# Kernel tuning notes

Measured on AMD Instinct MI355X. Metric: run time of the kernel, lower is better.

## Reference

```python
import jax, jax.numpy as jnp
import numpy as np

B, S, D, H = 2, 2048, 1024, 16
DK = D // H


def setup_inputs() -> dict:
    key = jax.random.key(0)
    ks = jax.random.split(key, 11)
    sc = 0.02
    return {
        "q": jax.random.normal(ks[0], (B, S, D), jnp.float32),
        "k": jax.random.normal(ks[1], (B, S, D), jnp.float32),
        "v": jax.random.normal(ks[2], (B, S, D), jnp.float32),
        "mask": jnp.ones((1, 1, S, S), jnp.int32),
        "w_q": jax.random.normal(ks[3], (D, D), jnp.float32) * sc,
        "b_q": jnp.zeros((D,), jnp.float32),
        "w_k": jax.random.normal(ks[4], (D, D), jnp.float32) * sc,
        "b_k": jnp.zeros((D,), jnp.float32),
        "w_v": jax.random.normal(ks[5], (D, D), jnp.float32) * sc,
        "b_v": jnp.zeros((D,), jnp.float32),
        "w_o": jax.random.normal(ks[6], (D, D), jnp.float32) * sc,
        "b_o": jnp.zeros((D,), jnp.float32),
    }


def reference(q, k, v, mask, w_q, b_q, w_k, b_k, w_v, b_v, w_o, b_o):
    # projections (torch Linear: x @ W.T + b)
    Q = q @ w_q.T + b_q
    K = k @ w_k.T + b_k
    V = v @ w_v.T + b_v
    # [B,S,D] -> [B,H,S,DK]
    Q = Q.reshape(B, S, H, DK).transpose(0, 2, 1, 3)
    K = K.reshape(B, S, H, DK).transpose(0, 2, 1, 3)
    V = V.reshape(B, S, H, DK).transpose(0, 2, 1, 3)
    scores = jnp.einsum('bhqd,bhkd->bhqk', Q, K) / jnp.sqrt(jnp.float32(DK))
    scores = jnp.where(mask == 0, jnp.float32(-1e9), scores)
    attn = jax.nn.softmax(scores, axis=-1)  # dropout p=0.0 -> identity
    X = jnp.einsum('bhqk,bhkd->bhqd', attn, V)
    X = X.transpose(0, 2, 1, 3).reshape(B, S, D)
    return X @ w_o.T + b_o
```

## Files before the change

### kernel.cpp

```cpp
#include <hip/hip_runtime.h>
#include <cstdint>
#include <cstddef>


typedef __attribute__((ext_vector_type(8))) short short8;
typedef __attribute__((ext_vector_type(4))) float float4v;
typedef __attribute__((ext_vector_type(4))) unsigned short us4;

#define DEV __device__ __forceinline__
#define MFMA16(a, b, c) __builtin_amdgcn_mfma_f32_16x16x32_bf16((a), (b), (c), 0, 0, 0)

DEV unsigned short f2bf(float f) {
  union { float f; unsigned u; } c; c.f = f;
  unsigned u = c.u + 0x7fffu + ((c.u >> 16) & 1u);
  return (unsigned short)(u >> 16);
}

DEV void async16(const void* g, void* l) {
  __builtin_amdgcn_global_load_lds(
      (__attribute__((address_space(1))) void*)(uintptr_t)g,
      (__attribute__((address_space(3))) void*)l, 16, 0, 0);
}

struct CvtJob { const float* src; unsigned short* dst; int n; int mode; };
struct CvtArgs { CvtJob job[8]; };

__global__ __launch_bounds__(256) void cvt_bf16_kernel(CvtArgs args) {
  CvtJob j = args.job[blockIdx.y];
  int i = (blockIdx.x * 256 + threadIdx.x) * 8;
  if (i >= j.n) return;
  if (j.mode == 0) {
    float4v a = *(const float4v*)(j.src + i);
    float4v b = *(const float4v*)(j.src + i + 4);
    short8 o;
#pragma unroll
    for (int t = 0; t < 4; ++t) { o[t] = (short)f2bf(a[t]); o[t + 4] = (short)f2bf(b[t]); }
    *(short8*)(j.dst + i) = o;
  } else {
    const int* mi = (const int*)j.src + i;
    int4 a = ((const int4*)mi)[0], b = ((const int4*)mi)[1];
    unsigned bits = (a.x != 0 ? 1u : 0) | (a.y != 0 ? 2u : 0) | (a.z != 0 ? 4u : 0) |
                    (a.w != 0 ? 8u : 0) | (b.x != 0 ? 16u : 0) | (b.y != 0 ? 32u : 0) |
                    (b.z != 0 ? 64u : 0) | (b.w != 0 ? 128u : 0);
    unsigned long long w = (unsigned long long)bits << ((threadIdx.x & 7) * 8);
    w |= __shfl_xor(w, 1);
    w |= __shfl_xor(w, 2);
    w |= __shfl_xor(w, 4);
    if ((threadIdx.x & 7) == 0) ((unsigned long long*)j.dst)[i >> 6] = w;
  }
}

__global__ __launch_bounds__(64) void mask_flags_kernel(const unsigned long long* __restrict__ mb,
                                                        unsigned int* __restrict__ flags) {
  int qb = blockIdx.x >> 5, kt = blockIdx.x & 31;
  unsigned long long w = mb[(size_t)(qb * 64 + threadIdx.x) * 32 + kt];
  unsigned long long b = __ballot(w == ~0ULL);
  if (threadIdx.x == 0) flags[blockIdx.x] = (b == ~0ULL) ? 1u : 0u;
}

struct GemmJob {
  const unsigned short* A; const unsigned short* W; const float* bias;
  void* out; float scale; int mode;
};
struct GemmArgs { GemmJob job[3]; };

__global__ __launch_bounds__(256, 2) void gemm128_kernel(GemmArgs args) {
  const GemmJob jb = args.job[blockIdx.z];
  const int tid = threadIdx.x;
  const int wave = tid >> 6, lane = tid & 63, lk = lane & 15, quad = lane >> 4;
  const int wm = wave >> 1, wn = wave & 1;
  const int m0 = blockIdx.y * 128, n0 = blockIdx.x * 128;

  __shared__ unsigned short As[128 * 32];
  __shared__ unsigned short Bs[128 * 32];

  float4v acc[4][4] = {};

  const char* Ag = (const char*)jb.A + (size_t)m0 * 2048;
  const char* Wg = (const char*)jb.W + (size_t)n0 * 2048;

#pragma unroll 1
  for (int kk = 0; kk < 32; ++kk) {
    __syncthreads();
    const int kbyte = kk * 64;
#pragma unroll
    for (int i = 0; i < 2; ++i) {
      int o = (wave * 2 + i) * 1024 + lane * 16;
      int r = o >> 6, cb = o & 63;
      async16(Ag + (size_t)r * 2048 + kbyte + cb, (char*)As + (wave * 2 + i) * 1024);
      async16(Wg + (size_t)r * 2048 + kbyte + cb, (char*)Bs + (wave * 2 + i) * 1024);
    }
    __builtin_amdgcn_s_waitcnt(0);
    __syncthreads();

    short8 af[4];
#pragma unroll
    for (int mt = 0; mt < 4; ++mt)
      af[mt] = *(const short8*)(&As[(wm * 64 + mt * 16 + lk) * 32 + quad * 8]);
#pragma unroll
    for (int nt = 0; nt < 4; ++nt) {
      short8 bf = *(const short8*)(&Bs[(wn * 64 + nt * 16 + lk) * 32 + quad * 8]);
#pragma unroll
      for (int mt = 0; mt < 4; ++mt)
        acc[mt][nt] = MFMA16(af[mt], bf, acc[mt][nt]);
    }
  }

  if (jb.mode == 0) {
    unsigned short* outp = (unsigned short*)jb.out;
#pragma unroll
    for (int nt = 0; nt < 4; ++nt) {
      int n = n0 + wn * 64 + nt * 16 + lk;
      float bn = jb.bias[n];
      int h = n >> 6, d = n & 63;
#pragma unroll
      for (int mt = 0; mt < 4; ++mt) {
#pragma unroll
        for (int r = 0; r < 4; ++r) {
          int m = m0 + wm * 64 + mt * 16 + quad * 4 + r;
          int b = m >> 11, s = m & 2047;
          float v = (acc[mt][nt][r] + bn) * jb.scale;
          outp[((size_t)((b * 16 + h) * 2048 + s) << 6) + d] = f2bf(v);
        }
      }
    }
  } else {
    unsigned short* outp = (unsigned short*)jb.out;
#pragma unroll
    for (int nt = 0; nt < 4; ++nt) {
      int n = n0 + wn * 64 + nt * 16 + lk;
      float bn = jb.bias[n];
      int h = n >> 6, d = n & 63;
#pragma unroll
      for (int mt = 0; mt < 4; ++mt) {
        int m = m0 + wm * 64 + mt * 16 + quad * 4;
        int b = m >> 11, s = m & 2047;
        us4 pk;
#pragma unroll
        for (int r = 0; r < 4; ++r) pk[r] = f2bf(acc[mt][nt][r] + bn);
        *(us4*)(&outp[((size_t)((b * 16 + h) * 64 + d) << 11) + s]) = pk;
      }
    }
  }
}

__global__ __launch_bounds__(256, 2) void gemm_out64_kernel(
    const unsigned short* __restrict__ A, const unsigned short* __restrict__ W,
    const float* __restrict__ bias, float* __restrict__ out) {
  const int tid = threadIdx.x;
  const int wave = tid >> 6, lane = tid & 63, lk = lane & 15, quad = lane >> 4;
  const int wm = wave >> 1, wn = wave & 1;
  const int m0 = blockIdx.y * 64, n0 = blockIdx.x * 128;

  __shared__ unsigned short As[64 * 32];
  __shared__ unsigned short Bs[128 * 32];

  float4v acc[2][4] = {};

  const char* Ag = (const char*)A + (size_t)m0 * 2048;
  const char* Wg = (const char*)W + (size_t)n0 * 2048;

#pragma unroll 1
  for (int kk = 0; kk < 32; ++kk) {
    __syncthreads();
    const int kbyte = kk * 64;
    {
      int o = wave * 1024 + lane * 16;
      int r = o >> 6, cb = o & 63;
      async16(Ag + (size_t)r * 2048 + kbyte + cb, (char*)As + wave * 1024);
    }
#pragma unroll
    for (int i = 0; i < 2; ++i) {
      int o = (wave * 2 + i) * 1024 + lane * 16;
      int r = o >> 6, cb = o & 63;
      async16(Wg + (size_t)r * 2048 + kbyte + cb, (char*)Bs + (wave * 2 + i) * 1024);
    }
    __builtin_amdgcn_s_waitcnt(0);
    __syncthreads();

    short8 af[2];
#pragma unroll
    for (int mt = 0; mt < 2; ++mt)
      af[mt] = *(const short8*)(&As[(wm * 32 + mt * 16 + lk) * 32 + quad * 8]);
#pragma unroll
    for (int nt = 0; nt < 4; ++nt) {
      short8 bf = *(const short8*)(&Bs[(wn * 64 + nt * 16 + lk) * 32 + quad * 8]);
#pragma unroll
      for (int mt = 0; mt < 2; ++mt)
        acc[mt][nt] = MFMA16(af[mt], bf, acc[mt][nt]);
    }
  }

#pragma unroll
  for (int nt = 0; nt < 4; ++nt) {
    int n = n0 + wn * 64 + nt * 16 + lk;
    float bn = bias[n];
#pragma unroll
    for (int mt = 0; mt < 2; ++mt) {
#pragma unroll
      for (int r = 0; r < 4; ++r) {
        int m = m0 + wm * 32 + mt * 16 + quad * 4 + r;
        out[(size_t)m * 1024 + n] = acc[mt][nt][r] + bn;
      }
    }
  }
}

__global__ __launch_bounds__(256, 4) void attn_kernel(
    const unsigned short* __restrict__ Qp, const unsigned short* __restrict__ Kp,
    const unsigned short* __restrict__ Vtp, const unsigned int* __restrict__ flags,
    const unsigned long long* __restrict__ mbits, unsigned short* __restrict__ Xout) {
  __shared__ unsigned short Qs[64 * 64];
  __shared__ unsigned short Ks[64 * 64];
  __shared__ unsigned short Vts[64 * 64];
  __shared__ unsigned short Ps[64 * 72];

  const int tid = threadIdx.x, wave = tid >> 6, lane = tid & 63;
  const int lk = lane & 15, quad = lane >> 4;
  const int bh = blockIdx.y, q0 = blockIdx.x * 64;
  const size_t cbase = (size_t)bh * (2048 * 64);
  const int r8 = lane >> 3, gs = lane & 7;
  const int sw = lk & 7;

#pragma unroll
  for (int i = 0; i < 2; ++i) {
    int row = wave * 16 + i * 8 + r8;
    int g = gs ^ (row & 7);
    async16(Qp + cbase + (size_t)(q0 + row) * 64 + g * 8,
            (char*)Qs + (wave * 16 + i * 8) * 128);
  }
  __builtin_amdgcn_s_waitcnt(0x0f70);

  short8 qf[2];
#pragma unroll
  for (int ks = 0; ks < 2; ++ks) {
    int row = wave * 16 + lk;
    int gg = (ks * 4 + quad) ^ (row & 7);
    qf[ks] = *(const short8*)(&Qs[row * 64 + gg * 8]);
  }

  float rsum = 0.f;
  float4v O[4] = {};

#pragma unroll 1
  for (int kt = 0; kt < 32; ++kt) {
    __syncthreads();
#pragma unroll
    for (int i = 0; i < 2; ++i) {
      int row = wave * 16 + i * 8 + r8;
      int g = gs ^ (row & 7);
      async16(Kp + cbase + (size_t)(kt * 64 + row) * 64 + g * 8,
              (char*)Ks + (wave * 16 + i * 8) * 128);
      async16(Vtp + cbase + (size_t)row * 2048 + kt * 64 + g * 8,
              (char*)Vts + (wave * 16 + i * 8) * 128);
    }
    __builtin_amdgcn_s_waitcnt(0x0f70);
    __syncthreads();

    float4v sacc[4] = {};
#pragma unroll
    for (int kt4 = 0; kt4 < 4; ++kt4) {
      int krow = kt4 * 16 + lk;
      short8 ka0 = *(const short8*)(&Ks[krow * 64 + ((quad) ^ sw) * 8]);
      short8 ka1 = *(const short8*)(&Ks[krow * 64 + ((4 + quad) ^ sw) * 8]);
      sacc[kt4] = MFMA16(ka0, qf[0], sacc[kt4]);
      sacc[kt4] = MFMA16(ka1, qf[1], sacc[kt4]);
    }

    if (__builtin_expect(flags[blockIdx.x * 32 + kt] == 0, 0)) {
      unsigned long long w = mbits[(size_t)(q0 + wave * 16 + lk) * 32 + kt];
#pragma unroll
      for (int kt4 = 0; kt4 < 4; ++kt4)
#pragma unroll
        for (int r = 0; r < 4; ++r)
          if (!((w >> (kt4 * 16 + quad * 4 + r)) & 1ULL))
            sacc[kt4][r] = -__builtin_inff();
    }

#pragma unroll
    for (int kt4 = 0; kt4 < 4; ++kt4) {
      us4 pk;
#pragma unroll
      for (int r = 0; r < 4; ++r) {
        float p = __expf(sacc[kt4][r]);
        unsigned pu = __float_as_uint(p);
        rsum += __uint_as_float(pu & 0xffff0000u);
        pk[r] = (unsigned short)(pu >> 16);
      }
      *(us4*)(&Ps[(wave * 16 + lk) * 72 + kt4 * 16 + quad * 4]) = pk;
    }

    short8 pa[2];
#pragma unroll
    for (int ks = 0; ks < 2; ++ks)
      pa[ks] = *(const short8*)(&Ps[(wave * 16 + lk) * 72 + ks * 32 + quad * 8]);
#pragma unroll
    for (int dt = 0; dt < 4; ++dt) {
      int drow = dt * 16 + lk;
      short8 vb0 = *(const short8*)(&Vts[drow * 64 + ((quad) ^ sw) * 8]);
      short8 vb1 = *(const short8*)(&Vts[drow * 64 + ((4 + quad) ^ sw) * 8]);
      O[dt] = MFMA16(pa[0], vb0, O[dt]);
      O[dt] = MFMA16(pa[1], vb1, O[dt]);
    }
  }

  float s = rsum;
  s += __shfl_xor(s, 16);
  s += __shfl_xor(s, 32);
  float inv = 1.f / s;
  float linv[4];
#pragma unroll
  for (int r = 0; r < 4; ++r) linv[r] = __shfl(inv, (wave << 6 & 0) + quad * 4 + r);

  const int b = bh >> 4, h = bh & 15;
#pragma unroll
  for (int dt = 0; dt < 4; ++dt)
#pragma unroll
    for (int r = 0; r < 4; ++r) {
      int qq = q0 + wave * 16 + quad * 4 + r;
      int d = dt * 16 + lk;
      Xout[((size_t)(b * 2048 + qq)) * 1024 + h * 64 + d] = f2bf(O[dt][r] * linv[r]);
    }
}

extern "C" void kernel_launch(void* const* d_in, const int* in_sizes, int n_in,
                              void* d_out, int out_size, void* d_ws, size_t ws_size,
                              hipStream_t stream) {
  const float* q   = (const float*)d_in[0];
  const float* k   = (const float*)d_in[1];
  const float* v   = (const float*)d_in[2];
  const int*   msk = (const int*)d_in[3];
  const float* w_q = (const float*)d_in[4];
  const float* b_q = (const float*)d_in[5];
  const float* w_k = (const float*)d_in[6];
  const float* b_k = (const float*)d_in[7];
  const float* w_v = (const float*)d_in[8];
  const float* b_v = (const float*)d_in[9];
  const float* w_o = (const float*)d_in[10];
  const float* b_o = (const float*)d_in[11];

  char* ws = (char*)d_ws;
  const size_t MB = (size_t)1 << 20;
  unsigned short* q_bf  = (unsigned short*)(ws + 0 * MB);
  unsigned short* k_bf  = (unsigned short*)(ws + 8 * MB);
  unsigned short* v_bf  = (unsigned short*)(ws + 16 * MB);
  unsigned short* wq_bf = (unsigned short*)(ws + 24 * MB);
  unsigned short* wk_bf = (unsigned short*)(ws + 26 * MB);
  unsigned short* wv_bf = (unsigned short*)(ws + 28 * MB);
  unsigned short* wo_bf = (unsigned short*)(ws + 30 * MB);
  unsigned short* Qp    = (unsigned short*)(ws + 32 * MB);
  unsigned short* Kp    = (unsigned short*)(ws + 40 * MB);
  unsigned short* Vtp   = (unsigned short*)(ws + 48 * MB);
  unsigned short* Xa    = (unsigned short*)(ws + 56 * MB);
  unsigned long long* mb = (unsigned long long*)(ws + 64 * MB);
  unsigned int* mflags   = (unsigned int*)(ws + 64 * MB + (512 << 10));

  CvtArgs ca;
  ca.job[0] = { q,   q_bf,  4096 * 1024, 0 };
  ca.job[1] = { k,   k_bf,  4096 * 1024, 0 };
  ca.job[2] = { v,   v_bf,  4096 * 1024, 0 };
  ca.job[3] = { w_q, wq_bf, 1024 * 1024, 0 };
  ca.job[4] = { w_k, wk_bf, 1024 * 1024, 0 };
  ca.job[5] = { w_v, wv_bf, 1024 * 1024, 0 };
  ca.job[6] = { w_o, wo_bf, 1024 * 1024, 0 };
  ca.job[7] = { (const float*)msk, (unsigned short*)mb, 2048 * 2048, 1 };
  cvt_bf16_kernel<<<dim3(2048, 8), 256, 0, stream>>>(ca);

  mask_flags_kernel<<<dim3(1024), 64, 0, stream>>>(mb, mflags);

  GemmArgs ga;
  ga.job[0] = { q_bf, wq_bf, b_q, (void*)Qp,  0.125f, 0 };
  ga.job[1] = { k_bf, wk_bf, b_k, (void*)Kp,  1.0f,   0 };
  ga.job[2] = { v_bf, wv_bf, b_v, (void*)Vtp, 1.0f,   2 };
  gemm128_kernel<<<dim3(8, 32, 3), 256, 0, stream>>>(ga);

  attn_kernel<<<dim3(32, 32), 256, 0, stream>>>(Qp, Kp, Vtp, mflags, mb, Xa);

  gemm_out64_kernel<<<dim3(8, 64), 256, 0, stream>>>(Xa, wo_bf, b_o, (float*)d_out);
}
```

Before: 247.7 us.

## Load K/V directly from global into MFMA fragments, remap blocks per XCD, use exp2

The attention kernel stops staging Q, K and V tiles through shared memory with async loads and two barriers per iteration. Each wave now reads its MFMA fragments straight from global memory and relies on the cache. Blocks are remapped so that all query blocks of a head land on the same XCD, which should improve L2 reuse of K/V. The softmax exponent switches to exp2 with log2(e) folded into the Q scale, and P is packed with the bf16x2 conversion intrinsic. Removing barriers trades against redundant global/L2 traffic, since the four waves each fetch the same K/V data.

```diff
diff --git a/kernel.cpp b/kernel.cpp
--- a/kernel.cpp
+++ b/kernel.cpp
@@ -1,4 +1,5 @@
 #include <hip/hip_runtime.h>
+#include <hip/hip_bf16.h>
 #include <cstdint>
 #include <cstddef>
 
@@ -14,6 +15,12 @@
   union { float f; unsigned u; } c; c.f = f;
   unsigned u = c.u + 0x7fffu + ((c.u >> 16) & 1u);
   return (unsigned short)(u >> 16);
+}
+
+DEV unsigned pkbf2(float a, float b) {
+  __hip_bfloat162 h = __float22bfloat162_rn(make_float2(a, b));
+  union { __hip_bfloat162 h; unsigned u; } c; c.h = h;
+  return c.u;
 }
 
 DEV void async16(const void* g, void* l) {
@@ -210,64 +217,42 @@
     const unsigned short* __restrict__ Qp, const unsigned short* __restrict__ Kp,
     const unsigned short* __restrict__ Vtp, const unsigned int* __restrict__ flags,
     const unsigned long long* __restrict__ mbits, unsigned short* __restrict__ Xout) {
-  __shared__ unsigned short Qs[64 * 64];
-  __shared__ unsigned short Ks[64 * 64];
-  __shared__ unsigned short Vts[64 * 64];
   __shared__ unsigned short Ps[64 * 72];
 
   const int tid = threadIdx.x, wave = tid >> 6, lane = tid & 63;
   const int lk = lane & 15, quad = lane >> 4;
-  const int bh = blockIdx.y, q0 = blockIdx.x * 64;
+
+  const int bid = blockIdx.y * 32 + blockIdx.x;
+  const int xcd = bid & 7, idx = bid >> 3;
+  const int bh = xcd * 4 + (idx >> 5);
+  const int qb = idx & 31, q0 = qb * 64;
   const size_t cbase = (size_t)bh * (2048 * 64);
-  const int r8 = lane >> 3, gs = lane & 7;
-  const int sw = lk & 7;
-
-#pragma unroll
-  for (int i = 0; i < 2; ++i) {
-    int row = wave * 16 + i * 8 + r8;
-    int g = gs ^ (row & 7);
-    async16(Qp + cbase + (size_t)(q0 + row) * 64 + g * 8,
-            (char*)Qs + (wave * 16 + i * 8) * 128);
-  }
-  __builtin_amdgcn_s_waitcnt(0x0f70);
-
+
+  const unsigned short* qrow = Qp + cbase + (size_t)(q0 + wave * 16 + lk) * 64 + quad * 8;
   short8 qf[2];
-#pragma unroll
-  for (int ks = 0; ks < 2; ++ks) {
-    int row = wave * 16 + lk;
-    int gg = (ks * 4 + quad) ^ (row & 7);
-    qf[ks] = *(const short8*)(&Qs[row * 64 + gg * 8]);
-  }
+  qf[0] = *(const short8*)(qrow);
+  qf[1] = *(const short8*)(qrow + 32);
+
+  const unsigned short* kbase = Kp + cbase + (size_t)lk * 64 + quad * 8;
+  const unsigned short* vbase = Vtp + cbase + (size_t)lk * 2048 + quad * 8;
+  unsigned short* psrow = &Ps[(wave * 16 + lk) * 72];
 
   float rsum = 0.f;
   float4v O[4] = {};
 
 #pragma unroll 1
   for (int kt = 0; kt < 32; ++kt) {
-    __syncthreads();
-#pragma unroll
-    for (int i = 0; i < 2; ++i) {
-      int row = wave * 16 + i * 8 + r8;
-      int g = gs ^ (row & 7);
-      async16(Kp + cbase + (size_t)(kt * 64 + row) * 64 + g * 8,
-              (char*)Ks + (wave * 16 + i * 8) * 128);
-      async16(Vtp + cbase + (size_t)row * 2048 + kt * 64 + g * 8,
-              (char*)Vts + (wave * 16 + i * 8) * 128);
-    }
-    __builtin_amdgcn_s_waitcnt(0x0f70);
-    __syncthreads();
-
     float4v sacc[4] = {};
 #pragma unroll
     for (int kt4 = 0; kt4 < 4; ++kt4) {
-      int krow = kt4 * 16 + lk;
-      short8 ka0 = *(const short8*)(&Ks[krow * 64 + ((quad) ^ sw) * 8]);
-      short8 ka1 = *(const short8*)(&Ks[krow * 64 + ((4 + quad) ^ sw) * 8]);
+      const unsigned short* kp = kbase + ((size_t)kt * 64 + kt4 * 16) * 64;
+      short8 ka0 = *(const short8*)(kp);
+      short8 ka1 = *(const short8*)(kp + 32);
       sacc[kt4] = MFMA16(ka0, qf[0], sacc[kt4]);
       sacc[kt4] = MFMA16(ka1, qf[1], sacc[kt4]);
     }
 
-    if (__builtin_expect(flags[blockIdx.x * 32 + kt] == 0, 0)) {
+    if (__builtin_expect(flags[qb * 32 + kt] == 0, 0)) {
       unsigned long long w = mbits[(size_t)(q0 + wave * 16 + lk) * 32 + kt];
 #pragma unroll
       for (int kt4 = 0; kt4 < 4; ++kt4)
@@ -279,28 +264,26 @@
 
 #pragma unroll
     for (int kt4 = 0; kt4 < 4; ++kt4) {
-      us4 pk;
-#pragma unroll
-      for (int r = 0; r < 4; ++r) {
-        float p = __expf(sacc[kt4][r]);
-        unsigned pu = __float_as_uint(p);
-        rsum += __uint_as_float(pu & 0xffff0000u);
-        pk[r] = (unsigned short)(pu >> 16);
-      }
-      *(us4*)(&Ps[(wave * 16 + lk) * 72 + kt4 * 16 + quad * 4]) = pk;
-    }
-
-    short8 pa[2];
-#pragma unroll
-    for (int ks = 0; ks < 2; ++ks)
-      pa[ks] = *(const short8*)(&Ps[(wave * 16 + lk) * 72 + ks * 32 + quad * 8]);
+      float p0 = __builtin_amdgcn_exp2f(sacc[kt4][0]);
+      float p1 = __builtin_amdgcn_exp2f(sacc[kt4][1]);
+      float p2 = __builtin_amdgcn_exp2f(sacc[kt4][2]);
+      float p3 = __builtin_amdgcn_exp2f(sacc[kt4][3]);
+      rsum += (p0 + p1) + (p2 + p3);
+      uint2 pk;
+      pk.x = pkbf2(p0, p1);
+      pk.y = pkbf2(p2, p3);
+      *(uint2*)(psrow + kt4 * 16 + quad * 4) = pk;
+    }
+
+    short8 pa0 = *(const short8*)(psrow + quad * 8);
+    short8 pa1 = *(const short8*)(psrow + 32 + quad * 8);
 #pragma unroll
     for (int dt = 0; dt < 4; ++dt) {
-      int drow = dt * 16 + lk;
-      short8 vb0 = *(const short8*)(&Vts[drow * 64 + ((quad) ^ sw) * 8]);
-      short8 vb1 = *(const short8*)(&Vts[drow * 64 + ((4 + quad) ^ sw) * 8]);
-      O[dt] = MFMA16(pa[0], vb0, O[dt]);
-      O[dt] = MFMA16(pa[1], vb1, O[dt]);
+      const unsigned short* vp = vbase + (size_t)dt * 16 * 2048 + (size_t)kt * 64;
+      short8 vb0 = *(const short8*)(vp);
+      short8 vb1 = *(const short8*)(vp + 32);
+      O[dt] = MFMA16(pa0, vb0, O[dt]);
+      O[dt] = MFMA16(pa1, vb1, O[dt]);
     }
   }
 
@@ -310,7 +293,7 @@
   float inv = 1.f / s;
   float linv[4];
 #pragma unroll
-  for (int r = 0; r < 4; ++r) linv[r] = __shfl(inv, (wave << 6 & 0) + quad * 4 + r);
+  for (int r = 0; r < 4; ++r) linv[r] = __shfl(inv, quad * 4 + r);
 
   const int b = bh >> 4, h = bh & 15;
 #pragma unroll
@@ -369,7 +352,7 @@
   mask_flags_kernel<<<dim3(1024), 64, 0, stream>>>(mb, mflags);
 
   GemmArgs ga;
-  ga.job[0] = { q_bf, wq_bf, b_q, (void*)Qp,  0.125f, 0 };
+  ga.job[0] = { q_bf, wq_bf, b_q, (void*)Qp,  0.1803368801111204f, 0 };
   ga.job[1] = { k_bf, wk_bf, b_k, (void*)Kp,  1.0f,   0 };
   ga.job[2] = { v_bf, wv_bf, b_v, (void*)Vtp, 1.0f,   2 };
   gemm128_kernel<<<dim3(8, 32, 3), 256, 0, stream>>>(ga);
```

Result: slower. 419.0 us (+69.1%).

## Use exp2 with log2e-folded Q scale, packed bf16 cvt, XCD-aware block remap

Applied to the files above, without the earlier changes.

Folds log2(e) into the Q projection scale so the softmax can use the native exp2 instruction instead of __expf. P values are now converted with round-to-nearest packed bf16 conversion, and the row sum uses the full fp32 values instead of the truncated ones. Attention blocks are also remapped so that all blocks of one (batch, head) land on the same XCD, which should improve L2 reuse of K/V. The numerics shift slightly, because the sum is no longer consistent with the bf16-rounded P.

```diff
diff --git a/kernel.cpp b/kernel.cpp
--- a/kernel.cpp
+++ b/kernel.cpp
@@ -1,4 +1,5 @@
 #include <hip/hip_runtime.h>
+#include <hip/hip_bf16.h>
 #include <cstdint>
 #include <cstddef>
 
@@ -14,6 +15,12 @@
   union { float f; unsigned u; } c; c.f = f;
   unsigned u = c.u + 0x7fffu + ((c.u >> 16) & 1u);
   return (unsigned short)(u >> 16);
+}
+
+DEV unsigned pkbf2(float a, float b) {
+  __hip_bfloat162 h = __float22bfloat162_rn(make_float2(a, b));
+  union { __hip_bfloat162 h; unsigned u; } c; c.h = h;
+  return c.u;
 }
 
 DEV void async16(const void* g, void* l) {
@@ -217,7 +224,11 @@
 
   const int tid = threadIdx.x, wave = tid >> 6, lane = tid & 63;
   const int lk = lane & 15, quad = lane >> 4;
-  const int bh = blockIdx.y, q0 = blockIdx.x * 64;
+
+  const int bid = blockIdx.y * 32 + blockIdx.x;
+  const int xcd = bid & 7, idx = bid >> 3;
+  const int bh = xcd * 4 + (idx >> 5);
+  const int qb = idx & 31, q0 = qb * 64;
   const size_t cbase = (size_t)bh * (2048 * 64);
   const int r8 = lane >> 3, gs = lane & 7;
   const int sw = lk & 7;
@@ -267,7 +278,7 @@
       sacc[kt4] = MFMA16(ka1, qf[1], sacc[kt4]);
     }
 
-    if (__builtin_expect(flags[blockIdx.x * 32 + kt] == 0, 0)) {
+    if (__builtin_expect(flags[qb * 32 + kt] == 0, 0)) {
       unsigned long long w = mbits[(size_t)(q0 + wave * 16 + lk) * 32 + kt];
 #pragma unroll
       for (int kt4 = 0; kt4 < 4; ++kt4)
@@ -279,15 +290,15 @@
 
 #pragma unroll
     for (int kt4 = 0; kt4 < 4; ++kt4) {
-      us4 pk;
-#pragma unroll
-      for (int r = 0; r < 4; ++r) {
-        float p = __expf(sacc[kt4][r]);
-        unsigned pu = __float_as_uint(p);
-        rsum += __uint_as_float(pu & 0xffff0000u);
-        pk[r] = (unsigned short)(pu >> 16);
-      }
-      *(us4*)(&Ps[(wave * 16 + lk) * 72 + kt4 * 16 + quad * 4]) = pk;
+      float p0 = __builtin_amdgcn_exp2f(sacc[kt4][0]);
+      float p1 = __builtin_amdgcn_exp2f(sacc[kt4][1]);
+      float p2 = __builtin_amdgcn_exp2f(sacc[kt4][2]);
+      float p3 = __builtin_amdgcn_exp2f(sacc[kt4][3]);
+      rsum += (p0 + p1) + (p2 + p3);
+      uint2 pk;
+      pk.x = pkbf2(p0, p1);
+      pk.y = pkbf2(p2, p3);
+      *(uint2*)(&Ps[(wave * 16 + lk) * 72 + kt4 * 16 + quad * 4]) = pk;
     }
 
     short8 pa[2];
@@ -310,7 +321,7 @@
   float inv = 1.f / s;
   float linv[4];
 #pragma unroll
-  for (int r = 0; r < 4; ++r) linv[r] = __shfl(inv, (wave << 6 & 0) + quad * 4 + r);
+  for (int r = 0; r < 4; ++r) linv[r] = __shfl(inv, quad * 4 + r);
 
   const int b = bh >> 4, h = bh & 15;
 #pragma unroll
@@ -369,7 +380,7 @@
   mask_flags_kernel<<<dim3(1024), 64, 0, stream>>>(mb, mflags);
 
   GemmArgs ga;
-  ga.job[0] = { q_bf, wq_bf, b_q, (void*)Qp,  0.125f, 0 };
+  ga.job[0] = { q_bf, wq_bf, b_q, (void*)Qp,  0.1803368801111204f, 0 };
   ga.job[1] = { k_bf, wk_bf, b_k, (void*)Kp,  1.0f,   0 };
   ga.job[2] = { v_bf, wv_bf, b_v, (void*)Vtp, 1.0f,   2 };
   gemm128_kernel<<<dim3(8, 32, 3), 256, 0, stream>>>(ga);
```

New measurement: 244.5 us. Within noise of the previous version (-1.3%).
